# Kernel tuning notes

Measured on AMD Instinct MI355X. Metric: run time of the kernel, lower is better.

## Reference

```python
import jax, jax.numpy as jnp
import numpy as np

RCR = 5.2          # radial cutoff
RCA = 3.5          # angular cutoff
ETA_R = 16.0
SHF_R = jnp.asarray(0.9 + 0.26875 * np.arange(16), jnp.float32)          # 16 radial shifts
ZETA = 32.0
SHF_Z = jnp.asarray((2 * np.arange(8) + 1) * np.pi / 16.0, jnp.float32)  # 8 angle shifts
ETA_A = 8.0
SHF_A = jnp.asarray(0.9 + 0.65 * np.arange(4), jnp.float32)              # 4 angular radial shifts
NUM_SPECIES = 4
NUM_PAIRS = NUM_SPECIES * (NUM_SPECIES + 1) // 2  # 10


def _pair_index_table():
    idx = np.zeros((NUM_SPECIES, NUM_SPECIES), np.int32)
    c = 0
    for s1 in range(NUM_SPECIES):
        for s2 in range(s1, NUM_SPECIES):
            idx[s1, s2] = c
            idx[s2, s1] = c
            c += 1
    return jnp.asarray(idx)

PAIR_IDX = _pair_index_table()


def _cutoff(d, rc):
    return jnp.where(d <= rc, 0.5 * jnp.cos(jnp.pi * d / rc) + 0.5, 0.0)


def setup_inputs() -> dict:
    key = jax.random.key(0)
    k1, k2 = jax.random.split(key)
    species = jax.random.randint(k1, (32, 48), 0, NUM_SPECIES, dtype=jnp.int32)
    coords = jax.random.uniform(k2, (32, 48, 3), jnp.float32) * 7.0  # 7 Angstrom box
    return {"species": species, "coords": coords}


def reference(species, coords):
    B, A = species.shape
    dt = coords.dtype
    # vec[b,i,j] = coords[j] - coords[i]
    diff = coords[:, None, :, :] - coords[:, :, None, :]           # [B,A,A,3]
    d2 = jnp.sum(diff * diff, -1)
    eye = jnp.eye(A, dtype=bool)
    dist = jnp.sqrt(jnp.where(eye, 1.0, d2))                        # safe on diagonal
    valid = (species[:, :, None] >= 0) & (species[:, None, :] >= 0) & (~eye)

    # ---------- radial AEV ----------
    fc_r = jnp.where(valid & (dist <= RCR), _cutoff(dist, RCR), 0.0)
    rad_terms = 0.25 * jnp.exp(-ETA_R * (dist[..., None] - SHF_R) ** 2) * fc_r[..., None]  # [B,A,A,16]
    sp_onehot = jax.nn.one_hot(jnp.clip(species, 0), NUM_SPECIES, dtype=dt)                # [B,A,4]
    radial = jnp.einsum('bijr,bjs->bisr', rad_terms, sp_onehot).reshape(B, A, NUM_SPECIES * 16)

    # ---------- angular AEV ----------
    in_ca = valid & (dist <= RCA)
    fc_a = jnp.where(in_ca, _cutoff(dist, RCA), 0.0)
    dotp = jnp.einsum('bijc,bikc->bijk', diff, diff)                # [B,A,A,A]
    cos_t = 0.95 * dotp / (dist[:, :, :, None] * dist[:, :, None, :])
    angles = jnp.arccos(cos_t)
    f1 = ((1.0 + jnp.cos(angles[..., None] - SHF_Z)) * 0.5) ** ZETA          # [B,A,A,A,8]
    avg_d = 0.5 * (dist[:, :, :, None] + dist[:, :, None, :])
    f2 = jnp.exp(-ETA_A * (avg_d[..., None] - SHF_A) ** 2)                   # [B,A,A,A,4]
    jk = jnp.triu(jnp.ones((A, A), bool), 1)                                 # unordered neighbor pairs j<k
    trip_mask = in_ca[:, :, :, None] & in_ca[:, :, None, :] & jk
    w = jnp.where(trip_mask, 2.0 * fc_a[:, :, :, None] * fc_a[:, :, None, :], 0.0)  # [B,A,A,A]
    pair_idx = PAIR_IDX[jnp.clip(species, 0)[:, :, None], jnp.clip(species, 0)[:, None, :]]  # [B,A,A]
    pair_oh = jax.nn.one_hot(pair_idx, NUM_PAIRS, dtype=dt)                  # [B,A,A,10]
    angular = jnp.einsum('bijk,bijka,bijkz,bjkp->bipaz', w, f2, f1, pair_oh)
    angular = angular.reshape(B, A, NUM_PAIRS * 4 * 8)

    aevs = jnp.concatenate([radial, angular], axis=-1)   # [B,A,384]
    return species, aevs
```

## Files before the change

### kernel.cpp

```cpp
#include <hip/hip_runtime.h>
#include <math.h>

#define NB 32
#define NA 48
#define RCRf 5.2f
#define RCAf 3.5f
#define PI_F 3.14159265358979f
#define CMAX 384

__device__ inline void tri_decode(int t, int m, int T, int& jj, int& kk) {
    const int u = T - 1 - t;
    int r = (int)((sqrtf(8.0f * (float)u + 1.0f) - 1.0f) * 0.5f);
    while (r * (r + 1) / 2 > u) --r;
    while ((r + 1) * (r + 2) / 2 <= u) ++r;
    jj = m - 2 - r;
    kk = m - 1 - (u - r * (r + 1) / 2);
}

__global__ __launch_bounds__(320)
void aev_kernel(const int* __restrict__ species, const float* __restrict__ coords,
                float* __restrict__ out)
{
    const int bid = blockIdx.x;
    const int b = bid / NA;
    const int i = bid - b * NA;
    const int tid = threadIdx.x;

    __shared__ float crd[NA * 3];
    __shared__ int   ssp[NA];
    __shared__ float pd[NA], pfr[NA];
    __shared__ float cdx[NA], cdy[NA], cdz[NA], cdd[NA], cfc[NA];
    __shared__ int   csp[NA];
    __shared__ int   sm;
    __shared__ float radpart[5 * 64];
    __shared__ __align__(16) float f1rec[CMAX * 8];
    __shared__ __align__(16) float w2rec[CMAX * 4];
    __shared__ int   trec[CMAX];
    __shared__ int   cnt[10];
    __shared__ unsigned cur[10];

    if (tid < NA * 3) crd[tid] = coords[(size_t)b * NA * 3 + tid];
    if (tid >= 192 && tid < 192 + NA) ssp[tid - 192] = species[b * NA + (tid - 192)];
    if (tid >= 256 && tid < 266) cnt[tid - 256] = 0;
    __syncthreads();

    const float xi = crd[3 * i], yi = crd[3 * i + 1], zi = crd[3 * i + 2];

    if (tid < 64) {
        const int j = tid;
        float dx = 0.f, dy = 0.f, dz = 0.f, d = 1.0f, fr = 0.0f, fa = 0.0f;
        bool inA = false;
        if (j < NA) {
            dx = crd[3 * j] - xi; dy = crd[3 * j + 1] - yi; dz = crd[3 * j + 2] - zi;
            d = sqrtf(dx * dx + dy * dy + dz * dz);
            if (j != i && d <= RCRf) fr = 0.5f * __cosf((PI_F / RCRf) * d) + 0.5f;
            if (j != i && d <= RCAf) { inA = true; fa = 0.5f * __cosf((PI_F / RCAf) * d) + 0.5f; }
            pd[j] = d; pfr[j] = fr;
        }
        const unsigned long long mask = __ballot(inA);
        if (inA) {
            const int pos = (int)__popcll(mask & ((1ull << j) - 1ull));
            cdx[pos] = dx; cdy[pos] = dy; cdz[pos] = dz;
            cdd[pos] = d;  cfc[pos] = fa; csp[pos] = ssp[j];
        }
        if (j == 0) sm = (int)__popcll(mask);
    }
    __syncthreads();

    const int m = sm;
    const int T = m * (m - 1) / 2;
    const int nchunks = (T + CMAX - 1) / CMAX;

    {
        const int f = tid & 63, seg = tid >> 6;
        const int s = f >> 4, r = f & 15;
        const float shf = 0.9f + 0.26875f * (float)r;
        float acc = 0.0f;
        const int j0 = seg * 10, j1 = min(NA, j0 + 10);
        for (int j = j0; j < j1; ++j) {
            const float fr = pfr[j];
            if (fr != 0.0f) {
                const float u = pd[j] - shf;
                const float v = 0.25f * __expf(-16.0f * u * u) * fr;
                acc += (ssp[j] == s) ? v : 0.0f;
            }
        }
        radpart[seg * 64 + f] = acc;
    }
    {
        const int cT = min(CMAX, T);
        for (int t = tid; t < cT; t += 320) {
            int jj, kk; tri_decode(t, m, T, jj, kk);
            const int s1 = csp[jj], s2 = csp[kk];
            const int lo = min(s1, s2), hi = max(s1, s2);
            const int p = (lo * (9 - lo)) / 2 + (hi - lo);
            trec[t] = jj | (kk << 6) | (p << 12);
            atomicAdd(&cnt[p], 1);
        }
    }
    __syncthreads();

    const float CZ[8] = { 0.98078528f, 0.83146961f, 0.55557023f, 0.19509032f,
                         -0.19509032f,-0.55557023f,-0.83146961f,-0.98078528f };
    const float SZ[8] = { 0.19509032f, 0.55557023f, 0.83146961f, 0.98078528f,
                          0.98078528f, 0.83146961f, 0.55557023f, 0.19509032f };
    const float SA[4] = { 0.9f, 1.55f, 2.2f, 2.85f };

    const int pmine = tid >> 5, amine = (tid >> 3) & 3, zmine = tid & 7;
    float acc_a = 0.0f;

    for (int c = 0; c < nchunks; ++c) {
        const int t0 = c * CMAX;
        const int cT = min(CMAX, T - t0);

        int mybase = 0, mycnt = 0, run = 0;
        #pragma unroll
        for (int p = 0; p < 10; ++p) {
            const int cp = cnt[p];
            if (p == pmine) { mybase = run; mycnt = cp; }
            if (tid < 10 && p == tid) cur[tid] = (unsigned)run;
            run += cp;
        }
        __syncthreads();

        for (int t = tid; t < cT; t += 320) {
            const int pk = trec[t];
            const int jj = pk & 63, kk = (pk >> 6) & 63, p = pk >> 12;

            const float djx = cdx[jj], djy = cdy[jj], djz = cdz[jj];
            const float dkx = cdx[kk], dky = cdy[kk], dkz = cdz[kk];
            const float dj = cdd[jj], dk = cdd[kk];
            const float dot = djx * dkx + djy * dky + djz * dkz;
            const float cosT = 0.95f * dot * __frcp_rn(dj * dk);
            const float sinT = sqrtf(fmaxf(1.0f - cosT * cosT, 0.0f));
            const float avg = 0.5f * (dj + dk);
            const float w = 2.0f * cfc[jj] * cfc[kk];

            float f1v[8];
            #pragma unroll
            for (int z = 0; z < 8; ++z) {
                const float base = 0.5f + 0.5f * (cosT * CZ[z] + sinT * SZ[z]);
                const float b2 = base * base, b4 = b2 * b2, b8 = b4 * b4, b16 = b8 * b8;
                f1v[z] = b16 * b16;
            }
            float w2v[4];
            #pragma unroll
            for (int a = 0; a < 4; ++a) {
                const float u = avg - SA[a];
                w2v[a] = w * __expf(-8.0f * u * u);
            }
            const unsigned pos = atomicAdd(&cur[p], 1u);
            ((float4*)f1rec)[pos * 2]     = make_float4(f1v[0], f1v[1], f1v[2], f1v[3]);
            ((float4*)f1rec)[pos * 2 + 1] = make_float4(f1v[4], f1v[5], f1v[6], f1v[7]);
            ((float4*)w2rec)[pos]         = make_float4(w2v[0], w2v[1], w2v[2], w2v[3]);
        }
        __syncthreads();

        for (int k = mybase; k < mybase + mycnt; ++k)
            acc_a += w2rec[k * 4 + amine] * f1rec[k * 8 + zmine];

        if (c + 1 < nchunks) {
            __syncthreads();
            if (tid < 10) cnt[tid] = 0;
            __syncthreads();
            const int n0 = (c + 1) * CMAX;
            const int nT = min(CMAX, T - n0);
            for (int t = tid; t < nT; t += 320) {
                int jj, kk; tri_decode(n0 + t, m, T, jj, kk);
                const int s1 = csp[jj], s2 = csp[kk];
                const int lo = min(s1, s2), hi = max(s1, s2);
                const int p = (lo * (9 - lo)) / 2 + (hi - lo);
                trec[t] = jj | (kk << 6) | (p << 12);
                atomicAdd(&cnt[p], 1);
            }
            __syncthreads();
        }
    }

    float* op = out + NB * NA + (size_t)(b * NA + i) * 384;
    if (tid < 64) {
        op[tid] = radpart[tid] + radpart[64 + tid] + radpart[128 + tid] +
                  radpart[192 + tid] + radpart[256 + tid];
    }
    op[64 + tid] = acc_a;
    if (tid == 0) out[b * NA + i] = (float)ssp[i];
}

extern "C" void kernel_launch(void* const* d_in, const int* in_sizes, int n_in,
                              void* d_out, int out_size, void* d_ws, size_t ws_size,
                              hipStream_t stream) {
    const int*   species = (const int*)d_in[0];
    const float* coords  = (const float*)d_in[1];
    float*       out     = (float*)d_out;
    aev_kernel<<<NB * NA, 320, 0, stream>>>(species, coords, out);
}
```

Baseline: 66.49 us.

## Store angular triple records in fp16 and process all triples in one pass

Per-triple f1 and w2 terms are now packed as fp16 into shared buffers big enough for every neighbor pair, so the chunk loop and its extra barriers go away. The packed index array is dropped: the triangle decode runs once when counting per species pair and again when computing terms. Neighbor displacement and distance are packed into one float4 to cut shared-memory loads. In exchange the kernel uses more LDS, which can lower occupancy, and fp16 storage loses precision, since the (base)^32 values can underflow.

```diff
diff --git a/kernel.cpp b/kernel.cpp
--- a/kernel.cpp
+++ b/kernel.cpp
@@ -6,9 +6,20 @@
 #define RCRf 5.2f
 #define RCAf 3.5f
 #define PI_F 3.14159265358979f
-#define CMAX 384
+#define TREC 1128
 
-__device__ inline void tri_decode(int t, int m, int T, int& jj, int& kk) {
+typedef unsigned short ushort_t;
+typedef __fp16 h2f __attribute__((ext_vector_type(2)));
+
+static __device__ __forceinline__ unsigned pkh(float a, float b) {
+    h2f v = __builtin_amdgcn_cvt_pkrtz(a, b);
+    return __builtin_bit_cast(unsigned, v);
+}
+static __device__ __forceinline__ float uph(ushort_t u) {
+    return (float)__builtin_bit_cast(__fp16, u);
+}
+
+static __device__ __forceinline__ void tri_decode(int t, int m, int T, int& jj, int& kk) {
     const int u = T - 1 - t;
     int r = (int)((sqrtf(8.0f * (float)u + 1.0f) - 1.0f) * 0.5f);
     while (r * (r + 1) / 2 > u) --r;
@@ -29,13 +40,13 @@
     __shared__ float crd[NA * 3];
     __shared__ int   ssp[NA];
     __shared__ float pd[NA], pfr[NA];
-    __shared__ float cdx[NA], cdy[NA], cdz[NA], cdd[NA], cfc[NA];
+    __shared__ __align__(16) float4 cpk[NA];
+    __shared__ float cfc[NA];
     __shared__ int   csp[NA];
     __shared__ int   sm;
     __shared__ float radpart[5 * 64];
-    __shared__ __align__(16) float f1rec[CMAX * 8];
-    __shared__ __align__(16) float w2rec[CMAX * 4];
-    __shared__ int   trec[CMAX];
+    __shared__ __align__(16) ushort_t f1h[TREC * 8];
+    __shared__ __align__(16) ushort_t w2h[TREC * 4];
     __shared__ int   cnt[10];
     __shared__ unsigned cur[10];
 
@@ -60,8 +71,8 @@
         const unsigned long long mask = __ballot(inA);
         if (inA) {
             const int pos = (int)__popcll(mask & ((1ull << j) - 1ull));
-            cdx[pos] = dx; cdy[pos] = dy; cdz[pos] = dz;
-            cdd[pos] = d;  cfc[pos] = fa; csp[pos] = ssp[j];
+            cpk[pos] = make_float4(dx, dy, dz, d);
+            cfc[pos] = fa; csp[pos] = ssp[j];
         }
         if (j == 0) sm = (int)__popcll(mask);
     }
@@ -69,7 +80,6 @@
 
     const int m = sm;
     const int T = m * (m - 1) / 2;
-    const int nchunks = (T + CMAX - 1) / CMAX;
 
     {
         const int f = tid & 63, seg = tid >> 6;
@@ -87,16 +97,23 @@
         }
         radpart[seg * 64 + f] = acc;
     }
-    {
-        const int cT = min(CMAX, T);
-        for (int t = tid; t < cT; t += 320) {
-            int jj, kk; tri_decode(t, m, T, jj, kk);
-            const int s1 = csp[jj], s2 = csp[kk];
-            const int lo = min(s1, s2), hi = max(s1, s2);
-            const int p = (lo * (9 - lo)) / 2 + (hi - lo);
-            trec[t] = jj | (kk << 6) | (p << 12);
-            atomicAdd(&cnt[p], 1);
-        }
+    for (int t = tid; t < T; t += 320) {
+        int jj, kk; tri_decode(t, m, T, jj, kk);
+        const int s1 = csp[jj], s2 = csp[kk];
+        const int lo = min(s1, s2), hi = max(s1, s2);
+        const int p = (lo * (9 - lo)) / 2 + (hi - lo);
+        atomicAdd(&cnt[p], 1);
+    }
+    __syncthreads();
+
+    const int pmine = tid >> 5, amine = (tid >> 3) & 3, zmine = tid & 7;
+    int mybase = 0, mycnt = 0, run = 0;
+    #pragma unroll
+    for (int p = 0; p < 10; ++p) {
+        const int cp = cnt[p];
+        if (p == pmine) { mybase = run; mycnt = cp; }
+        if (tid < 10 && p == tid) cur[tid] = (unsigned)run;
+        run += cp;
     }
     __syncthreads();
 
@@ -106,76 +123,46 @@
                           0.98078528f, 0.83146961f, 0.55557023f, 0.19509032f };
     const float SA[4] = { 0.9f, 1.55f, 2.2f, 2.85f };
 
-    const int pmine = tid >> 5, amine = (tid >> 3) & 3, zmine = tid & 7;
+    for (int t = tid; t < T; t += 320) {
+        int jj, kk; tri_decode(t, m, T, jj, kk);
+        const float4 qj = cpk[jj];
+        const float4 qk = cpk[kk];
+        const float dot = qj.x * qk.x + qj.y * qk.y + qj.z * qk.z;
+        const float cosT = 0.95f * dot * __frcp_rn(qj.w * qk.w);
+        const float sinT = sqrtf(fmaxf(1.0f - cosT * cosT, 0.0f));
+        const float avg = 0.5f * (qj.w + qk.w);
+        const float w = 2.0f * cfc[jj] * cfc[kk];
+        const int s1 = csp[jj], s2 = csp[kk];
+        const int lo = min(s1, s2), hi = max(s1, s2);
+        const int p = (lo * (9 - lo)) / 2 + (hi - lo);
+
+        float f1v[8];
+        #pragma unroll
+        for (int z = 0; z < 8; ++z) {
+            const float base = 0.5f + 0.5f * (cosT * CZ[z] + sinT * SZ[z]);
+            const float b2 = base * base, b4 = b2 * b2, b8 = b4 * b4, b16 = b8 * b8;
+            f1v[z] = b16 * b16;
+        }
+        float w2v[4];
+        #pragma unroll
+        for (int a = 0; a < 4; ++a) {
+            const float u = avg - SA[a];
+            w2v[a] = w * __expf(-8.0f * u * u);
+        }
+        const unsigned pos = atomicAdd(&cur[p], 1u);
+        uint4 rf;
+        rf.x = pkh(f1v[0], f1v[1]); rf.y = pkh(f1v[2], f1v[3]);
+        rf.z = pkh(f1v[4], f1v[5]); rf.w = pkh(f1v[6], f1v[7]);
+        ((uint4*)f1h)[pos] = rf;
+        uint2 rw;
+        rw.x = pkh(w2v[0], w2v[1]); rw.y = pkh(w2v[2], w2v[3]);
+        ((uint2*)w2h)[pos] = rw;
+    }
+    __syncthreads();
+
     float acc_a = 0.0f;
-
-    for (int c = 0; c < nchunks; ++c) {
-        const int t0 = c * CMAX;
-        const int cT = min(CMAX, T - t0);
-
-        int mybase = 0, mycnt = 0, run = 0;
-        #pragma unroll
-        for (int p = 0; p < 10; ++p) {
-            const int cp = cnt[p];
-            if (p == pmine) { mybase = run; mycnt = cp; }
-            if (tid < 10 && p == tid) cur[tid] = (unsigned)run;
-            run += cp;
-        }
-        __syncthreads();
-
-        for (int t = tid; t < cT; t += 320) {
-            const int pk = trec[t];
-            const int jj = pk & 63, kk = (pk >> 6) & 63, p = pk >> 12;
-
-            const float djx = cdx[jj], djy = cdy[jj], djz = cdz[jj];
-            const float dkx = cdx[kk], dky = cdy[kk], dkz = cdz[kk];
-            const float dj = cdd[jj], dk = cdd[kk];
-            const float dot = djx * dkx + djy * dky + djz * dkz;
-            const float cosT = 0.95f * dot * __frcp_rn(dj * dk);
-            const float sinT = sqrtf(fmaxf(1.0f - cosT * cosT, 0.0f));
-            const float avg = 0.5f * (dj + dk);
-            const float w = 2.0f * cfc[jj] * cfc[kk];
-
-            float f1v[8];
-            #pragma unroll
-            for (int z = 0; z < 8; ++z) {
-                const float base = 0.5f + 0.5f * (cosT * CZ[z] + sinT * SZ[z]);
-                const float b2 = base * base, b4 = b2 * b2, b8 = b4 * b4, b16 = b8 * b8;
-                f1v[z] = b16 * b16;
-            }
-            float w2v[4];
-            #pragma unroll
-            for (int a = 0; a < 4; ++a) {
-                const float u = avg - SA[a];
-                w2v[a] = w * __expf(-8.0f * u * u);
-            }
-            const unsigned pos = atomicAdd(&cur[p], 1u);
-            ((float4*)f1rec)[pos * 2]     = make_float4(f1v[0], f1v[1], f1v[2], f1v[3]);
-            ((float4*)f1rec)[pos * 2 + 1] = make_float4(f1v[4], f1v[5], f1v[6], f1v[7]);
-            ((float4*)w2rec)[pos]         = make_float4(w2v[0], w2v[1], w2v[2], w2v[3]);
-        }
-        __syncthreads();
-
-        for (int k = mybase; k < mybase + mycnt; ++k)
-            acc_a += w2rec[k * 4 + amine] * f1rec[k * 8 + zmine];
-
-        if (c + 1 < nchunks) {
-            __syncthreads();
-            if (tid < 10) cnt[tid] = 0;
-            __syncthreads();
-            const int n0 = (c + 1) * CMAX;
-            const int nT = min(CMAX, T - n0);
-            for (int t = tid; t < nT; t += 320) {
-                int jj, kk; tri_decode(n0 + t, m, T, jj, kk);
-                const int s1 = csp[jj], s2 = csp[kk];
-                const int lo = min(s1, s2), hi = max(s1, s2);
-                const int p = (lo * (9 - lo)) / 2 + (hi - lo);
-                trec[t] = jj | (kk << 6) | (p << 12);
-                atomicAdd(&cnt[p], 1);
-            }
-            __syncthreads();
-        }
-    }
+    for (int k = mybase; k < mybase + mycnt; ++k)
+        acc_a += uph(w2h[k * 4 + amine]) * uph(f1h[k * 8 + zmine]);
 
     float* op = out + NB * NA + (size_t)(b * NA + i) * 384;
     if (tid < 64) {
```

Result: no change. 66.03 us (-0.7%).
